# Performance work log

Hardware: AMD Instinct MI355X
Metric: run time of the kernel (lower is better)

## Reference

```python
import jax, jax.numpy as jnp
import numpy as np

B, S, E, H, V = 1024, 64, 100, 512, 50000


def _gru_backward_last(x, wih, whh, bih, bhh):
    # x: [B,S,E]; PyTorch GRU cell, reverse direction; return final hidden [B,H]
    def step(h, xt):
        gi = xt @ wih.T + bih          # [B,3H]
        gh = h @ whh.T + bhh           # [B,3H]
        ir, iz, i_n = jnp.split(gi, 3, axis=-1)
        hr, hz, h_n = jnp.split(gh, 3, axis=-1)
        r = jax.nn.sigmoid(ir + hr)
        z = jax.nn.sigmoid(iz + hz)
        n = jnp.tanh(i_n + r * h_n)
        return (1.0 - z) * n + z * h, None
    h0 = jnp.zeros((x.shape[0], whh.shape[1]), x.dtype)
    hT, _ = jax.lax.scan(step, h0, x.transpose(1, 0, 2), reverse=True)
    return hT


def _encode(tokens, emb, wih, whh, bih, bhh):
    return _gru_backward_last(emb[tokens], wih, whh, bih, bhh)


def setup_inputs() -> dict:
    key = jax.random.key(0)
    ks = jax.random.split(key, 32)
    d = {}
    d['query'] = jax.random.randint(ks[0], (B, S), 0, V)
    d['context'] = jax.random.randint(ks[1], (B, S), 0, V)
    d['reply'] = jax.random.randint(ks[2], (B, S), 0, V)
    i = 3
    for tag in ('q', 'c', 'r'):
        d[f'emb_{tag}'] = jax.random.uniform(ks[i], (V, E), jnp.float32, -0.25, 0.25); i += 1
        d[f'wih_{tag}'] = jax.random.normal(ks[i], (3 * H, E), jnp.float32) * 0.05; i += 1
        d[f'whh_{tag}'] = jax.random.normal(ks[i], (3 * H, H), jnp.float32) * 0.05; i += 1
        d[f'bih_{tag}'] = jnp.zeros((3 * H,), jnp.float32); i += 1
        d[f'bhh_{tag}'] = jnp.zeros((3 * H,), jnp.float32); i += 1
    d['lin_w'] = jax.random.normal(ks[i], (H, H), jnp.float32) * 0.02
    d['lin_b'] = jnp.zeros((H,), jnp.float32)
    return d


def reference(query, context, reply,
              emb_q, wih_q, whh_q, bih_q, bhh_q,
              emb_c, wih_c, whh_c, bih_c, bhh_c,
              emb_r, wih_r, whh_r, bih_r, bhh_r,
              lin_w, lin_b):
    eq = _encode(query, emb_q, wih_q, whh_q, bih_q, bhh_q)    # [B,H]
    ec = _encode(context, emb_c, wih_c, whh_c, bih_c, bhh_c)  # [B,H]
    er = _encode(reply, emb_r, wih_r, whh_r, bih_r, bhh_r)    # [B,H]
    eqc = ((eq + ec) * 0.5) @ lin_w.T + lin_b                  # [B,H]
    sim = lambda a: jax.nn.softmax(a @ er.T, axis=-1)          # [B,B]
    return sim(eq), sim(ec), sim(eqc)
```

## Files before the change

### kernel.cpp

```cpp
#include <hip/hip_runtime.h>

typedef unsigned short u16;
typedef __attribute__((ext_vector_type(8))) short short8;
typedef __attribute__((ext_vector_type(4))) float f32x4;

#define B_   1024
#define S_   64
#define E_   100
#define H_   512
#define G3_  1536
#define XW_  256
#define WSZG (32 * 3 * 40 * 512)
#define GS_  (40 * 512)

typedef __attribute__((address_space(1))) const unsigned int gu32;
typedef __attribute__((address_space(3))) unsigned int lu32;

__device__ __forceinline__ float bf2f(u16 u) {
    union { unsigned int u; float f; } c; c.u = ((unsigned int)u) << 16; return c.f;
}
__device__ __forceinline__ u16 f2bf(float f) {
    union { float f; unsigned int u; } c; c.f = f;
    unsigned int r = c.u + 0x7fffu + ((c.u >> 16) & 1u);
    return (u16)(r >> 16);
}
__device__ __forceinline__ f32x4 mfma16(short8 a, short8 b, f32x4 c) {
    return __builtin_amdgcn_mfma_f32_16x16x32_bf16(a, b, c, 0, 0, 0);
}

__global__ __launch_bounds__(256) void gather_kernel(
    const int* __restrict__ tok, const float* __restrict__ emb, u16* __restrict__ xs)
{
    int tid = threadIdx.x;
    int hw  = tid & 31;
    int rowid = blockIdx.x * 8 + (tid >> 5);
    int t = rowid >> 10, b = rowid & 1023;
    int token = tok[b * S_ + t];
    const float* src = emb + (long)token * E_;
    u16* dst = xs + (long)rowid * XW_;
    int c0 = hw * 4;
    u16 a1[4], a2[4];
    #pragma unroll
    for (int j = 0; j < 4; ++j) {
        int c = c0 + j;
        float v = (c < E_) ? src[c] : 0.f;
        u16 h = f2bf(v);
        a1[j] = h;
        a2[j] = f2bf(v - bf2f(h));
    }
    uint2 p1, p2;
    p1.x = (unsigned)a1[0] | ((unsigned)a1[1] << 16);
    p1.y = (unsigned)a1[2] | ((unsigned)a1[3] << 16);
    p2.x = (unsigned)a2[0] | ((unsigned)a2[1] << 16);
    p2.y = (unsigned)a2[2] | ((unsigned)a2[3] << 16);
    *(uint2*)(dst + c0)       = p1;
    *(uint2*)(dst + 128 + c0) = p2;
}

__global__ __launch_bounds__(256) void repack_swz(
    const float* __restrict__ wih, const float* __restrict__ whh, u16* __restrict__ out)
{
    long idx = (long)blockIdx.x * 256 + threadIdx.x;
    int jj   = idx & 7;
    int lane = (idx >> 3) & 63;
    int q9   = (int)(idx >> 9);
    int ks   = q9 % 40;
    int q    = q9 / 40;
    int gate = q % 3;
    int ht   = q / 3;
    int n   = ht * 16 + (lane & 15);
    int ck  = (lane >> 4) * 8 + jj;
    int row = gate * H_ + n;
    float w; int lo;
    if (ks < 8) {
        int kk = (ks & 3) * 32 + ck;
        if (kk >= E_) { out[idx] = 0; return; }
        w = wih[row * E_ + kk];
        lo = (ks >> 2);
    } else {
        int rel = ks - 8;
        int kk  = (rel & 15) * 32 + ck;
        w = whh[row * H_ + kk];
        lo = (rel >> 4);
    }
    u16 h = f2bf(w);
    if (lo) h = f2bf(w - bf2f(h));
    out[idx] = h;
}

__global__ __launch_bounds__(256) void repack_lin(
    const float* __restrict__ lw, u16* __restrict__ l1, u16* __restrict__ l2)
{
    int i = blockIdx.x * 256 + threadIdx.x;
    float w = lw[i];
    u16 h = f2bf(w);
    l1[i] = h;
    l2[i] = f2bf(w - bf2f(h));
}

struct BiasPtrs { const float* bih[3]; const float* bhh[3]; };

__global__ __launch_bounds__(256, 3) void gru_step(
    const u16* __restrict__ xs,
    const u16* __restrict__ wswz,
    BiasPtrs bp,
    const u16* __restrict__ h1_in, const u16* __restrict__ h2_in,
    u16* __restrict__ h1_out, u16* __restrict__ h2_out,
    int t)
{
    __shared__ __attribute__((aligned(16))) u16 As[2][2][64 * 64];
    const int tid = threadIdx.x;
    const int lane = tid & 63;
    const int wid = tid >> 6;
    const int kh = tid >> 7;
    const int nh = (tid >> 6) & 1;
    const int l15 = lane & 15, l4 = lane >> 4;
    const int htp = blockIdx.x;
    const int m0  = blockIdx.y * 64;
    const int g   = blockIdx.z;
    const int ht  = htp * 2 + nh;

    const u16* wg  = wswz + (long)g * WSZG + (long)ht * (3 * GS_) + lane * 8;
    const u16* xb  = xs + ((long)(g * S_ + t) * B_ + m0) * XW_;
    const u16* hb1 = h1_in + ((long)g * B_ + m0) * H_;
    const u16* hb2 = h2_in + ((long)g * B_ + m0) * H_;

    f32x4 zero = {0.f, 0.f, 0.f, 0.f};
    f32x4 acc_r[4]  = {zero, zero, zero, zero};
    f32x4 acc_z[4]  = {zero, zero, zero, zero};
    f32x4 acc_ni[4] = {zero, zero, zero, zero};
    f32x4 acc_nh[4] = {zero, zero, zero, zero};

    auto stage_async = [&](int buf, const u16* s0, const u16* s1, int stride) {
        #pragma unroll
        for (int i = 0; i < 4; ++i) {
            int seg  = wid * 4 + i;
            int slot = seg >> 3;
            int rblk = seg & 7;
            const u16* src = slot ? s1 : s0;
            int row = rblk * 8 + (lane >> 3);
            int ch  = (lane & 7) ^ ((lane >> 3) & 7);
            const u16* gp = src + (long)row * stride + ch * 8;
            u16* lp = &As[buf][slot][rblk * 8 * 64];
            __builtin_amdgcn_global_load_lds((gu32*)gp, (lu32*)lp, 16, 0, 0);
        }
    };
    auto ldA = [&](const u16* sp, int ksl, int q) -> short8 {
        int r = q * 16 + l15;
        int p = ((ksl << 2) + l4) ^ (l15 & 7);
        return *(const short8*)(&sp[r * 64 + p * 8]);
    };
    auto consume_dual = [&](int buf, const u16* b1, const u16* b2, f32x4* accn) {
        const u16* sp = &As[buf][kh][0];
        #pragma unroll
        for (int ksl = 0; ksl < 2; ++ksl) {
            short8 br1 = *(const short8*)(b1 + ksl * 512);
            short8 bz1 = *(const short8*)(b1 + GS_ + ksl * 512);
            short8 bn1 = *(const short8*)(b1 + 2 * GS_ + ksl * 512);
            short8 br2 = *(const short8*)(b2 + ksl * 512);
            short8 bz2 = *(const short8*)(b2 + GS_ + ksl * 512);
            short8 bn2 = *(const short8*)(b2 + 2 * GS_ + ksl * 512);
            short8 a[4];
            #pragma unroll
            for (int q = 0; q < 4; ++q) a[q] = ldA(sp, ksl, q);
            #pragma unroll
            for (int q = 0; q < 4; ++q) {
                acc_r[q] = mfma16(a[q], br1, acc_r[q]);
                acc_z[q] = mfma16(a[q], bz1, acc_z[q]);
                accn[q]  = mfma16(a[q], bn1, accn[q]);
                acc_r[q] = mfma16(a[q], br2, acc_r[q]);
                acc_z[q] = mfma16(a[q], bz2, acc_z[q]);
                accn[q]  = mfma16(a[q], bn2, accn[q]);
            }
        }
    };
    auto consume_single = [&](int buf, const u16* b1, f32x4* accn) {
        const u16* sp = &As[buf][kh][0];
        #pragma unroll
        for (int ksl = 0; ksl < 2; ++ksl) {
            short8 br1 = *(const short8*)(b1 + ksl * 512);
            short8 bz1 = *(const short8*)(b1 + GS_ + ksl * 512);
            short8 bn1 = *(const short8*)(b1 + 2 * GS_ + ksl * 512);
            short8 a[4];
            #pragma unroll
            for (int q = 0; q < 4; ++q) a[q] = ldA(sp, ksl, q);
            #pragma unroll
            for (int q = 0; q < 4; ++q) {
                acc_r[q] = mfma16(a[q], br1, acc_r[q]);
                acc_z[q] = mfma16(a[q], bz1, acc_z[q]);
                accn[q]  = mfma16(a[q], bn1, accn[q]);
            }
        }
    };

    stage_async(0, xb, xb + 64, XW_);
    __syncthreads();
    stage_async(1, xb + 128, xb + 192, XW_);
    consume_dual(0, wg + (2 * kh) * 512, wg + (4 + 2 * kh) * 512, acc_ni);
    __syncthreads();
    stage_async(0, hb1, hb1 + 4 * 64, H_);
    consume_single(1, wg + (2 * kh) * 512, acc_ni);
    __syncthreads();
    stage_async(1, hb1 + 1 * 64, hb1 + 5 * 64, H_);
    consume_dual(0, wg + (8 + 8 * kh + 0) * 512, wg + (24 + 8 * kh + 0) * 512, acc_nh);
    __syncthreads();
    stage_async(0, hb1 + 2 * 64, hb1 + 6 * 64, H_);
    consume_dual(1, wg + (8 + 8 * kh + 2) * 512, wg + (24 + 8 * kh + 2) * 512, acc_nh);
    __syncthreads();
    stage_async(1, hb1 + 3 * 64, hb1 + 7 * 64, H_);
    consume_dual(0, wg + (8 + 8 * kh + 4) * 512, wg + (24 + 8 * kh + 4) * 512, acc_nh);
    __syncthreads();
    stage_async(0, hb2, hb2 + 4 * 64, H_);
    consume_dual(1, wg + (8 + 8 * kh + 6) * 512, wg + (24 + 8 * kh + 6) * 512, acc_nh);
    __syncthreads();
    stage_async(1, hb2 + 1 * 64, hb2 + 5 * 64, H_);
    consume_single(0, wg + (8 + 8 * kh + 0) * 512, acc_nh);
    __syncthreads();
    stage_async(0, hb2 + 2 * 64, hb2 + 6 * 64, H_);
    consume_single(1, wg + (8 + 8 * kh + 2) * 512, acc_nh);
    __syncthreads();
    stage_async(1, hb2 + 3 * 64, hb2 + 7 * 64, H_);
    consume_single(0, wg + (8 + 8 * kh + 4) * 512, acc_nh);
    __syncthreads();
    consume_single(1, wg + (8 + 8 * kh + 6) * 512, acc_nh);

    f32x4* rp = (f32x4*)As;
    const int rbase = (nh * 64 + lane) * 8;
    const int rxor  = lane & 7;
    if (kh == 1) {
        #pragma unroll
        for (int q = 0; q < 4; ++q) {
            rp[rbase + (q ^ rxor)]       = acc_r[q];
            rp[rbase + ((4 + q) ^ rxor)] = acc_z[q];
        }
    }
    __syncthreads();
    if (kh == 0) {
        #pragma unroll
        for (int q = 0; q < 4; ++q) {
            acc_r[q] += rp[rbase + (q ^ rxor)];
            acc_z[q] += rp[rbase + ((4 + q) ^ rxor)];
        }
    }
    __syncthreads();
    if (kh == 1) {
        #pragma unroll
        for (int q = 0; q < 4; ++q) {
            rp[rbase + (q ^ rxor)]       = acc_ni[q];
            rp[rbase + ((4 + q) ^ rxor)] = acc_nh[q];
        }
    }
    __syncthreads();
    if (kh == 0) {
        #pragma unroll
        for (int q = 0; q < 4; ++q) {
            acc_ni[q] += rp[rbase + (q ^ rxor)];
            acc_nh[q] += rp[rbase + ((4 + q) ^ rxor)];
        }

        int hc = ht * 16 + l15;
        const float* bih = bp.bih[g];
        const float* bhh = bp.bhh[g];
        float b_ir = bih[hc],          b_hr = bhh[hc];
        float b_iz = bih[H_ + hc],     b_hz = bhh[H_ + hc];
        float b_in = bih[2 * H_ + hc], b_hn = bhh[2 * H_ + hc];
        #pragma unroll
        for (int mt = 0; mt < 4; ++mt) {
            #pragma unroll
            for (int i = 0; i < 4; ++i) {
                int m = m0 + mt * 16 + l4 * 4 + i;
                long idx = ((long)g * B_ + m) * H_ + hc;
                float pr = acc_r[mt][i] + b_ir + b_hr;
                float pz = acc_z[mt][i] + b_iz + b_hz;
                float vi = acc_ni[mt][i] + b_in;
                float vh = acc_nh[mt][i] + b_hn;
                float r = 1.f / (1.f + __expf(-pr));
                float z = 1.f / (1.f + __expf(-pz));
                float n = tanhf(vi + r * vh);
                float hold = bf2f(h1_in[idx]) + bf2f(h2_in[idx]);
                float hnew = (1.f - z) * n + z * hold;
                u16 hh = f2bf(hnew);
                h1_out[idx] = hh;
                h2_out[idx] = f2bf(hnew - bf2f(hh));
            }
        }
    }
}

__global__ __launch_bounds__(256) void qc_kernel(
    const u16* __restrict__ h1, const u16* __restrict__ h2,
    u16* __restrict__ q1, u16* __restrict__ q2)
{
    int i = blockIdx.x * 256 + threadIdx.x;
    float eq = bf2f(h1[i]) + bf2f(h2[i]);
    float ec = bf2f(h1[B_ * H_ + i]) + bf2f(h2[B_ * H_ + i]);
    float q = 0.5f * (eq + ec);
    u16 h = f2bf(q);
    q1[i] = h;
    q2[i] = f2bf(q - bf2f(h));
}

struct GArgs { const u16* a[24]; const u16* b[24]; };

__global__ __launch_bounds__(256) void gemm_nt(
    GArgs ga, int nch, int astr, int bstr,
    const float* __restrict__ bias, float* __restrict__ outf,
    u16* __restrict__ ohi, u16* __restrict__ olo, int ldc, int mode)
{
    __shared__ __attribute__((aligned(16))) u16 As[64 * 72];
    __shared__ __attribute__((aligned(16))) u16 Bs[64 * 72];
    const int tid = threadIdx.x;
    const int w = tid >> 6, lane = tid & 63;
    const int l15 = lane & 15, l4 = lane >> 4;
    const int m0 = blockIdx.x * 64, n0 = blockIdx.y * 64;

    f32x4 zero = {0.f, 0.f, 0.f, 0.f};
    f32x4 acc[4] = {zero, zero, zero, zero};

    for (int c = 0; c < nch; ++c) {
        int row = tid >> 2, seg = tid & 3;
        const u16* sa = ga.a[c] + (long)(m0 + row) * astr + seg * 16;
        *(uint4*)(&As[row * 72 + seg * 16])     = *(const uint4*)(sa);
        *(uint4*)(&As[row * 72 + seg * 16 + 8]) = *(const uint4*)(sa + 8);
        const u16* sb = ga.b[c] + (long)(n0 + row) * bstr + seg * 16;
        *(uint4*)(&Bs[row * 72 + seg * 16])     = *(const uint4*)(sb);
        *(uint4*)(&Bs[row * 72 + seg * 16 + 8]) = *(const uint4*)(sb + 8);
        __syncthreads();
        #pragma unroll
        for (int ks = 0; ks < 2; ++ks) {
            short8 bfrag = *(const short8*)(&Bs[(w * 16 + l15) * 72 + ks * 32 + l4 * 8]);
            #pragma unroll
            for (int rt = 0; rt < 4; ++rt) {
                short8 a = *(const short8*)(&As[(rt * 16 + l15) * 72 + ks * 32 + l4 * 8]);
                acc[rt] = mfma16(a, bfrag, acc[rt]);
            }
        }
        __syncthreads();
    }

    int n = n0 + w * 16 + l15;
    float bv = bias ? bias[n] : 0.f;
    #pragma unroll
    for (int rt = 0; rt < 4; ++rt) {
        #pragma unroll
        for (int i = 0; i < 4; ++i) {
            int m = m0 + rt * 16 + l4 * 4 + i;
            float v = acc[rt][i] + bv;
            if (mode == 0) {
                outf[(long)m * ldc + n] = v;
            } else {
                u16 h = f2bf(v);
                ohi[(long)m * ldc + n] = h;
                olo[(long)m * ldc + n] = f2bf(v - bf2f(h));
            }
        }
    }
}

__global__ __launch_bounds__(256) void softmax_kernel(
    const float* __restrict__ lg, float* __restrict__ out)
{
    __shared__ float red[256];
    int row = blockIdx.x, tid = threadIdx.x;
    const float* src = lg + (long)row * 1024;
    float x[4];
    float mx = -1e30f;
    #pragma unroll
    for (int i = 0; i < 4; ++i) { x[i] = src[tid + 256 * i]; mx = fmaxf(mx, x[i]); }
    red[tid] = mx; __syncthreads();
    for (int s = 128; s > 0; s >>= 1) { if (tid < s) red[tid] = fmaxf(red[tid], red[tid + s]); __syncthreads(); }
    mx = red[0]; __syncthreads();
    float sm = 0.f;
    #pragma unroll
    for (int i = 0; i < 4; ++i) { x[i] = __expf(x[i] - mx); sm += x[i]; }
    red[tid] = sm; __syncthreads();
    for (int s = 128; s > 0; s >>= 1) { if (tid < s) red[tid] += red[tid + s]; __syncthreads(); }
    float inv = 1.f / red[0];
    float* dst = out + (long)row * 1024;
    #pragma unroll
    for (int i = 0; i < 4; ++i) dst[tid + 256 * i] = x[i] * inv;
}

extern "C" void kernel_launch(void* const* d_in, const int* in_sizes, int n_in,
                              void* d_out, int out_size, void* d_ws, size_t ws_size,
                              hipStream_t stream)
{
    const int* tok[3] = {(const int*)d_in[0], (const int*)d_in[1], (const int*)d_in[2]};
    const float *emb[3], *wih[3], *whh[3], *bih[3], *bhh[3];
    for (int g = 0; g < 3; ++g) {
        emb[g] = (const float*)d_in[3 + 5 * g];
        wih[g] = (const float*)d_in[4 + 5 * g];
        whh[g] = (const float*)d_in[5 + 5 * g];
        bih[g] = (const float*)d_in[6 + 5 * g];
        bhh[g] = (const float*)d_in[7 + 5 * g];
    }
    const float* lin_w = (const float*)d_in[18];
    const float* lin_b = (const float*)d_in[19];

    char* ws = (char*)d_ws;
    size_t off = 0;
    auto alloc = [&](size_t bytes) { void* p = ws + off; off += (bytes + 255) & ~255ull; return p; };

    const size_t BH  = (size_t)B_ * H_;
    const size_t PRB = 3 * BH * 2;
    const size_t PING = 2 * PRB;

    u16*   Xs   = (u16*)alloc(3ll * S_ * B_ * XW_ * 2);
    u16*   Wswz = (u16*)alloc(3ll * WSZG * 2);
    u16*   LW1  = (u16*)alloc((size_t)H_ * H_ * 2);
    u16*   LW2  = (u16*)alloc((size_t)H_ * H_ * 2);
    char*  HB   = (char*)alloc(2 * PING);
    u16*   QC1  = (u16*)alloc(BH * 2);
    u16*   QC2  = (u16*)alloc(BH * 2);
    u16*   EQ1  = (u16*)alloc(BH * 2);
    u16*   EQ2  = (u16*)alloc(BH * 2);
    float* LG   = (float*)alloc(3ll * B_ * B_ * 4);

    u16* H1[2]; u16* H2[2];
    for (int i = 0; i < 2; ++i) {
        char* pb = HB + (size_t)i * PING;
        H1[i] = (u16*)pb;
        H2[i] = (u16*)(pb + PRB);
    }

    hipMemsetAsync(HB, 0, PING, stream);

    for (int g = 0; g < 3; ++g) {
        gather_kernel<<<dim3(S_ * B_ / 8), 256, 0, stream>>>(tok[g], emb[g], Xs + (size_t)g * S_ * B_ * XW_);
        repack_swz<<<dim3(WSZG / 256), 256, 0, stream>>>(wih[g], whh[g], Wswz + (size_t)g * WSZG);
    }
    repack_lin<<<dim3(H_ * H_ / 256), 256, 0, stream>>>(lin_w, LW1, LW2);

    BiasPtrs bp;
    for (int g = 0; g < 3; ++g) { bp.bih[g] = bih[g]; bp.bhh[g] = bhh[g]; }

    int p = 0;
    for (int t = S_ - 1; t >= 0; --t) {
        gru_step<<<dim3(16, 16, 3), 256, 0, stream>>>(Xs, Wswz, bp,
            H1[p], H2[p], H1[1 - p], H2[1 - p], t);
        p ^= 1;
    }
    const u16* H1F = H1[p];
    const u16* H2F = H2[p];

    qc_kernel<<<dim3(BH / 256), 256, 0, stream>>>(H1F, H2F, QC1, QC2);

    GArgs ga;
    for (int c = 0; c < 8; ++c)   { ga.a[c] = QC1 + c * 64;        ga.b[c] = LW1 + c * 64; }
    for (int c = 8; c < 16; ++c)  { ga.a[c] = QC2 + (c - 8) * 64;  ga.b[c] = LW1 + (c - 8) * 64; }
    for (int c = 16; c < 24; ++c) { ga.a[c] = QC1 + (c - 16) * 64; ga.b[c] = LW2 + (c - 16) * 64; }
    gemm_nt<<<dim3(16, 8), 256, 0, stream>>>(ga, 24, H_, H_, lin_b, nullptr, EQ1, EQ2, H_, 1);

    const u16* R1 = H1F + 2 * BH;
    const u16* R2 = H2F + 2 * BH;
    for (int g = 0; g < 3; ++g) {
        const u16 *A1, *A2;
        if (g == 0)      { A1 = H1F;      A2 = H2F; }
        else if (g == 1) { A1 = H1F + BH; A2 = H2F + BH; }
        else             { A1 = EQ1;      A2 = EQ2; }
        GArgs gs;
        for (int c = 0; c < 8; ++c)   { gs.a[c] = A1 + c * 64;        gs.b[c] = R1 + c * 64; }
        for (int c = 8; c < 16; ++c)  { gs.a[c] = A2 + (c - 8) * 64;  gs.b[c] = R1 + (c - 8) * 64; }
        for (int c = 16; c < 24; ++c) { gs.a[c] = A1 + (c - 16) * 64; gs.b[c] = R2 + (c - 16) * 64; }
        gemm_nt<<<dim3(16, 16), 256, 0, stream>>>(gs, 24, H_, H_, nullptr,
            LG + (size_t)g * B_ * B_, nullptr, nullptr, B_, 0);
    }

    softmax_kernel<<<dim3(3 * B_), 256, 0, stream>>>(LG, (float*)d_out);
}
```

Measured before the change: 2.121 ms.

## Prefetch weight fragments a stage ahead and merge split-K reduction passes

Weight (B) fragments for the next MFMA stage are now loaded into registers before each barrier, so their global-load latency overlaps the current stage's compute and the async LDS staging. The two-round cross-wave reduction of the r/z and n accumulators becomes a single round using a larger LDS region, which removes two barriers. This raises register pressure (12 extra short8 values held live) and needs the reduction scratch to fit in the As buffer, with an added barrier before reuse.

```diff
diff --git a/kernel.cpp b/kernel.cpp
--- a/kernel.cpp
+++ b/kernel.cpp
@@ -8,7 +8,6 @@
 #define S_   64
 #define E_   100
 #define H_   512
-#define G3_  1536
 #define XW_  256
 #define WSZG (32 * 3 * 40 * 512)
 #define GS_  (40 * 512)
@@ -131,6 +130,27 @@
     f32x4 acc_ni[4] = {zero, zero, zero, zero};
     f32x4 acc_nh[4] = {zero, zero, zero, zero};
 
+    short8 pb[12];
+    auto loadB_dual = [&](const u16* b1, const u16* b2) {
+        #pragma unroll
+        for (int ksl = 0; ksl < 2; ++ksl) {
+            pb[ksl * 6 + 0] = *(const short8*)(b1 + ksl * 512);
+            pb[ksl * 6 + 1] = *(const short8*)(b1 + GS_ + ksl * 512);
+            pb[ksl * 6 + 2] = *(const short8*)(b1 + 2 * GS_ + ksl * 512);
+            pb[ksl * 6 + 3] = *(const short8*)(b2 + ksl * 512);
+            pb[ksl * 6 + 4] = *(const short8*)(b2 + GS_ + ksl * 512);
+            pb[ksl * 6 + 5] = *(const short8*)(b2 + 2 * GS_ + ksl * 512);
+        }
+    };
+    auto loadB_single = [&](const u16* b1) {
+        #pragma unroll
+        for (int ksl = 0; ksl < 2; ++ksl) {
+            pb[ksl * 6 + 0] = *(const short8*)(b1 + ksl * 512);
+            pb[ksl * 6 + 1] = *(const short8*)(b1 + GS_ + ksl * 512);
+            pb[ksl * 6 + 2] = *(const short8*)(b1 + 2 * GS_ + ksl * 512);
+        }
+    };
+
     auto stage_async = [&](int buf, const u16* s0, const u16* s1, int stride) {
         #pragma unroll
         for (int i = 0; i < 4; ++i) {
@@ -150,112 +170,102 @@
         int p = ((ksl << 2) + l4) ^ (l15 & 7);
         return *(const short8*)(&sp[r * 64 + p * 8]);
     };
-    auto consume_dual = [&](int buf, const u16* b1, const u16* b2, f32x4* accn) {
+    auto mfma_dual = [&](int buf, f32x4* accn) {
         const u16* sp = &As[buf][kh][0];
         #pragma unroll
         for (int ksl = 0; ksl < 2; ++ksl) {
-            short8 br1 = *(const short8*)(b1 + ksl * 512);
-            short8 bz1 = *(const short8*)(b1 + GS_ + ksl * 512);
-            short8 bn1 = *(const short8*)(b1 + 2 * GS_ + ksl * 512);
-            short8 br2 = *(const short8*)(b2 + ksl * 512);
-            short8 bz2 = *(const short8*)(b2 + GS_ + ksl * 512);
-            short8 bn2 = *(const short8*)(b2 + 2 * GS_ + ksl * 512);
             short8 a[4];
             #pragma unroll
             for (int q = 0; q < 4; ++q) a[q] = ldA(sp, ksl, q);
             #pragma unroll
             for (int q = 0; q < 4; ++q) {
-                acc_r[q] = mfma16(a[q], br1, acc_r[q]);
-                acc_z[q] = mfma16(a[q], bz1, acc_z[q]);
-                accn[q]  = mfma16(a[q], bn1, accn[q]);
-                acc_r[q] = mfma16(a[q], br2, acc_r[q]);
-                acc_z[q] = mfma16(a[q], bz2, acc_z[q]);
-                accn[q]  = mfma16(a[q], bn2, accn[q]);
+                acc_r[q] = mfma16(a[q], pb[ksl * 6 + 0], acc_r[q]);
+                acc_z[q] = mfma16(a[q], pb[ksl * 6 + 1], acc_z[q]);
+                accn[q]  = mfma16(a[q], pb[ksl * 6 + 2], accn[q]);
+                acc_r[q] = mfma16(a[q], pb[ksl * 6 + 3], acc_r[q]);
+                acc_z[q] = mfma16(a[q], pb[ksl * 6 + 4], acc_z[q]);
+                accn[q]  = mfma16(a[q], pb[ksl * 6 + 5], accn[q]);
             }
         }
     };
-    auto consume_single = [&](int buf, const u16* b1, f32x4* accn) {
+    auto mfma_single = [&](int buf, f32x4* accn) {
         const u16* sp = &As[buf][kh][0];
         #pragma unroll
         for (int ksl = 0; ksl < 2; ++ksl) {
-            short8 br1 = *(const short8*)(b1 + ksl * 512);
-            short8 bz1 = *(const short8*)(b1 + GS_ + ksl * 512);
-            short8 bn1 = *(const short8*)(b1 + 2 * GS_ + ksl * 512);
             short8 a[4];
             #pragma unroll
             for (int q = 0; q < 4; ++q) a[q] = ldA(sp, ksl, q);
             #pragma unroll
             for (int q = 0; q < 4; ++q) {
-                acc_r[q] = mfma16(a[q], br1, acc_r[q]);
-                acc_z[q] = mfma16(a[q], bz1, acc_z[q]);
-                accn[q]  = mfma16(a[q], bn1, accn[q]);
+                acc_r[q] = mfma16(a[q], pb[ksl * 6 + 0], acc_r[q]);
+                acc_z[q] = mfma16(a[q], pb[ksl * 6 + 1], acc_z[q]);
+                accn[q]  = mfma16(a[q], pb[ksl * 6 + 2], accn[q]);
             }
         }
     };
 
     stage_async(0, xb, xb + 64, XW_);
+    loadB_dual(wg + (2 * kh) * 512, wg + (4 + 2 * kh) * 512);
     __syncthreads();
     stage_async(1, xb + 128, xb + 192, XW_);
-    consume_dual(0, wg + (2 * kh) * 512, wg + (4 + 2 * kh) * 512, acc_ni);
+    mfma_dual(0, acc_ni);
+    loadB_single(wg + (2 * kh) * 512);
     __syncthreads();
     stage_async(0, hb1, hb1 + 4 * 64, H_);
-    consume_single(1, wg + (2 * kh) * 512, acc_ni);
+    mfma_single(1, acc_ni);
+    loadB_dual(wg + (8 + 8 * kh + 0) * 512, wg + (24 + 8 * kh + 0) * 512);
     __syncthreads();
     stage_async(1, hb1 + 1 * 64, hb1 + 5 * 64, H_);
-    consume_dual(0, wg + (8 + 8 * kh + 0) * 512, wg + (24 + 8 * kh + 0) * 512, acc_nh);
+    mfma_dual(0, acc_nh);
+    loadB_dual(wg + (8 + 8 * kh + 2) * 512, wg + (24 + 8 * kh + 2) * 512);
     __syncthreads();
     stage_async(0, hb1 + 2 * 64, hb1 + 6 * 64, H_);
-    consume_dual(1, wg + (8 + 8 * kh + 2) * 512, wg + (24 + 8 * kh + 2) * 512, acc_nh);
+    mfma_dual(1, acc_nh);
+    loadB_dual(wg + (8 + 8 * kh + 4) * 512, wg + (24 + 8 * kh + 4) * 512);
     __syncthreads();
     stage_async(1, hb1 + 3 * 64, hb1 + 7 * 64, H_);
-    consume_dual(0, wg + (8 + 8 * kh + 4) * 512, wg + (24 + 8 * kh + 4) * 512, acc_nh);
+    mfma_dual(0, acc_nh);
+    loadB_dual(wg + (8 + 8 * kh + 6) * 512, wg + (24 + 8 * kh + 6) * 512);
     __syncthreads();
     stage_async(0, hb2, hb2 + 4 * 64, H_);
-    consume_dual(1, wg + (8 + 8 * kh + 6) * 512, wg + (24 + 8 * kh + 6) * 512, acc_nh);
+    mfma_dual(1, acc_nh);
+    loadB_single(wg + (8 + 8 * kh + 0) * 512);
     __syncthreads();
     stage_async(1, hb2 + 1 * 64, hb2 + 5 * 64, H_);
-    consume_single(0, wg + (8 + 8 * kh + 0) * 512, acc_nh);
+    mfma_single(0, acc_nh);
+    loadB_single(wg + (8 + 8 * kh + 2) * 512);
     __syncthreads();
     stage_async(0, hb2 + 2 * 64, hb2 + 6 * 64, H_);
-    consume_single(1, wg + (8 + 8 * kh + 2) * 512, acc_nh);
+    mfma_single(1, acc_nh);
+    loadB_single(wg + (8 + 8 * kh + 4) * 512);
     __syncthreads();
     stage_async(1, hb2 + 3 * 64, hb2 + 7 * 64, H_);
-    consume_single(0, wg + (8 + 8 * kh + 4) * 512, acc_nh);
-    __syncthreads();
-    consume_single(1, wg + (8 + 8 * kh + 6) * 512, acc_nh);
-
+    mfma_single(0, acc_nh);
+    loadB_single(wg + (8 + 8 * kh + 6) * 512);
+    __syncthreads();
+    mfma_single(1, acc_nh);
+
+    __syncthreads();
     f32x4* rp = (f32x4*)As;
-    const int rbase = (nh * 64 + lane) * 8;
+    const int rbase = (nh * 64 + lane) * 16;
     const int rxor  = lane & 7;
     if (kh == 1) {
         #pragma unroll
         for (int q = 0; q < 4; ++q) {
-            rp[rbase + (q ^ rxor)]       = acc_r[q];
-            rp[rbase + ((4 + q) ^ rxor)] = acc_z[q];
+            rp[rbase + (q ^ rxor)]           = acc_r[q];
+            rp[rbase + ((4 + q) ^ rxor)]     = acc_z[q];
+            rp[rbase + 8 + (q ^ rxor)]       = acc_ni[q];
+            rp[rbase + 8 + ((4 + q) ^ rxor)] = acc_nh[q];
         }
     }
     __syncthreads();
     if (kh == 0) {
         #pragma unroll
         for (int q = 0; q < 4; ++q) {
-            acc_r[q] += rp[rbase + (q ^ rxor)];
-            acc_z[q] += rp[rbase + ((4 + q) ^ rxor)];
-        }
-    }
-    __syncthreads();
-    if (kh == 1) {
-        #pragma unroll
-        for (int q = 0; q < 4; ++q) {
-            rp[rbase + (q ^ rxor)]       = acc_ni[q];
-            rp[rbase + ((4 + q) ^ rxor)] = acc_nh[q];
-        }
-    }
-    __syncthreads();
-    if (kh == 0) {
-        #pragma unroll
-        for (int q = 0; q < 4; ++q) {
-            acc_ni[q] += rp[rbase + (q ^ rxor)];
-            acc_nh[q] += rp[rbase + ((4 + q) ^ rxor)];
+            acc_r[q]  += rp[rbase + (q ^ rxor)];
+            acc_z[q]  += rp[rbase + ((4 + q) ^ rxor)];
+            acc_ni[q] += rp[rbase + 8 + (q ^ rxor)];
+            acc_nh[q] += rp[rbase + 8 + ((4 + q) ^ rxor)];
         }
 
         int hc = ht * 16 + l15;
```

After: 2.203 ms. +3.9%, slower.
